# Optimization experiments

Hardware: AMD Instinct MI355X
Metric: run time of the kernel (lower is better)

## Reference

```python
import jax, jax.numpy as jnp
import numpy as np

B = 512        # graphs per batch
N_NODES = 64   # nodes per graph
IN_CH = 256
EMBED = 64
TOPK = 20
NEG_SLOPE = 0.2


def setup_inputs() -> dict:
    key = jax.random.key(0)
    ks = jax.random.split(key, 6)
    N = B * N_NODES
    x = jax.random.normal(ks[0], (N, IN_CH), dtype=jnp.float32)
    # fully-connected graph WITH self loops, per graph, sorted source-major
    src = jnp.repeat(jnp.arange(N_NODES, dtype=jnp.int32), N_NODES)  # [n*n]
    dst = jnp.tile(jnp.arange(N_NODES, dtype=jnp.int32), N_NODES)    # [n*n]
    offs = (jnp.arange(B, dtype=jnp.int32) * N_NODES)[:, None]       # [B,1]
    l = (src[None, :] + offs).reshape(-1)
    r = (dst[None, :] + offs).reshape(-1)
    edge_index = jnp.stack([l, r]).astype(jnp.int32)                 # [2, B*n*n]
    batch = jnp.repeat(jnp.arange(B, dtype=jnp.int32), N_NODES)      # [N]
    glorot = lambda k, sh: jax.random.uniform(k, sh, jnp.float32,
                                              -1.0, 1.0) * np.sqrt(6.0 / (sh[0] + sh[-1]))
    Wl = glorot(ks[1], (EMBED, IN_CH))
    bl = jnp.zeros((EMBED,), jnp.float32)
    Wr = glorot(ks[2], (EMBED, IN_CH))
    br = jnp.zeros((EMBED,), jnp.float32)
    att = glorot(ks[3], (1, EMBED))
    return {"x": x, "edge_index": edge_index, "batch": batch,
            "Wl": Wl, "bl": bl, "Wr": Wr, "br": br, "att": att}


def reference(x, edge_index, batch, Wl, bl, Wr, br, att):
    N = x.shape[0]
    x_l = x @ Wl.T + bl                      # [N, D]
    x_r = x @ Wr.T + br                      # [N, D]
    l, r = edge_index[0], edge_index[1]
    # edge gather + GAT-style score
    e = jax.nn.leaky_relu(x_l[l] + x_r[r], negative_slope=NEG_SLOPE)  # [E, D]
    alpha = (e * att[0]).sum(axis=-1)                                  # [E]
    # segment softmax grouped by source node l (each group is non-empty)
    m = jax.ops.segment_max(alpha, l, num_segments=N)
    a = jnp.exp(alpha - m[l])
    s = jax.ops.segment_sum(a, l, num_segments=N)
    a = a / s[l]
    # kNN sparsify: zero the diagonal then per-row topk
    a3 = a.reshape(B, N_NODES, N_NODES)
    a3 = a3 * (1.0 - jnp.eye(N_NODES, dtype=a3.dtype))
    attention, indices = jax.lax.top_k(a3, TOPK)     # [B, n, k] sorted desc
    attention = attention.reshape(-1)                 # [B*n*k]
    offs = (jnp.arange(B, dtype=jnp.int32) * N_NODES)[:, None]
    index_i = (jnp.repeat(jnp.arange(N_NODES, dtype=jnp.int32), TOPK)[None, :]
               + offs).reshape(-1)
    index_j = (indices.astype(jnp.int32)
               + (jnp.arange(B, dtype=jnp.int32) * N_NODES)[:, None, None]).reshape(-1)
    new_edge_index = jnp.stack([index_i, index_j])    # [2, B*n*k]
    return new_edge_index, attention
```

## Files before the change

kernel.cpp:

```cpp
#include <hip/hip_runtime.h>
#include <stdint.h>

#define NGRAPH 512
#define NN 64
#define INCH 256
#define DD 64
#define TOPK 20
#define XS 68
#define EPR 655360

typedef __attribute__((ext_vector_type(8))) short bf16x8;
typedef __attribute__((ext_vector_type(4))) float f32x4;

static __device__ __forceinline__ uint32_t f2bfbits(float f) {
  uint32_t u = __float_as_uint(f);
  return (u + 0x7FFFu + ((u >> 16) & 1u)) >> 16;
}
static __device__ __forceinline__ uint32_t pk2(float a, float b) {
  return f2bfbits(a) | (f2bfbits(b) << 16);
}

__global__ __launch_bounds__(256) void gat_fused(
    const float* __restrict__ x,
    const float* __restrict__ Wl,
    const float* __restrict__ blv,
    const float* __restrict__ Wr,
    const float* __restrict__ brv,
    const float* __restrict__ att,
    float* __restrict__ out)
{
  __shared__ __align__(16) uint8_t smem[65536];
  __shared__ float attL[DD];
  __shared__ float Sl[NN], Sr[NN];

  uint32_t* Bsh = (uint32_t*)smem;
  float* xlT  = (float*)smem;
  float* xrT  = (float*)(smem + 17408);
  float* alfT = (float*)(smem + 34816);

  const int b    = blockIdx.x;
  const int t    = threadIdx.x;
  const int w    = t >> 6;
  const int lane = t & 63;
  const int quad = lane >> 4;
  const int lo   = lane & 15;
  const int nodeBase = b * NN;

  {
    const int row  = t >> 1;
    const int half = t & 1;
    const float* src = (row < 64) ? (Wl + row * INCH) : (Wr + (row - 64) * INCH);
    uint4* BshV = (uint4*)Bsh;
    #pragma unroll
    for (int q = 0; q < 16; ++q) {
      const int kb = half * 16 + q;
      float4 a = *(const float4*)(src + kb * 8);
      float4 c = *(const float4*)(src + kb * 8 + 4);
      uint4 v = { pk2(a.x, a.y), pk2(a.z, a.w), pk2(c.x, c.y), pk2(c.z, c.w) };
      BshV[row * 32 + (kb ^ (row & 7))] = v;
    }
    if (t < DD) attL[t] = att[t];
  }
  __syncthreads();

  f32x4 acc[8];
  #pragma unroll
  for (int ct = 0; ct < 8; ++ct) acc[ct] = (f32x4){0.f, 0.f, 0.f, 0.f};

  const int r0 = w * 16;
  const uint4* BshV = (const uint4*)Bsh;
  #pragma unroll
  for (int ks = 0; ks < 8; ++ks) {
    const float* ap = x + (size_t)(nodeBase + r0 + lo) * INCH + ks * 32 + quad * 8;
    float4 a0 = *(const float4*)ap;
    float4 a1 = *(const float4*)(ap + 4);
    uint4 au = { pk2(a0.x, a0.y), pk2(a0.z, a0.w), pk2(a1.x, a1.y), pk2(a1.z, a1.w) };
    bf16x8 afrag = __builtin_bit_cast(bf16x8, au);
    #pragma unroll
    for (int ct = 0; ct < 8; ++ct) {
      const int n = (ct & 3) * 16 + lo + ((ct >= 4) ? 64 : 0);
      const int blk = (ks * 4 + quad) ^ (n & 7);
      uint4 bu = BshV[n * 32 + blk];
      bf16x8 bfrag = __builtin_bit_cast(bf16x8, bu);
      acc[ct] = __builtin_amdgcn_mfma_f32_16x16x32_bf16(afrag, bfrag, acc[ct], 0, 0, 0);
    }
  }
  __syncthreads();

  #pragma unroll
  for (int ct = 0; ct < 8; ++ct) {
    const int c = (ct & 3) * 16 + lo;
    const float bias = (ct < 4) ? blv[c] : brv[c];
    float* dstT = (ct < 4) ? xlT : xrT;
    #pragma unroll
    for (int r = 0; r < 4; ++r) {
      const int node = r0 + quad * 4 + r;
      dstT[c * XS + node] = acc[ct][r] + bias;
    }
  }
  __syncthreads();

  if (t < 64) {
    float s = 0.f;
    for (int d = 0; d < DD; ++d) s = fmaf(attL[d], xlT[d * XS + t], s);
    Sl[t] = s;
  } else if (t < 128) {
    const int i = t - 64;
    float s = 0.f;
    for (int d = 0; d < DD; ++d) s = fmaf(attL[d], xrT[d * XS + i], s);
    Sr[i] = s;
  }

  const int i0 = (t >> 4) * 4;
  const int j0 = (t & 15) * 4;
  float pacc[4][4];
  #pragma unroll
  for (int a = 0; a < 4; ++a)
    #pragma unroll
    for (int c = 0; c < 4; ++c) pacc[a][c] = 0.f;

  for (int d = 0; d < DD; ++d) {
    f32x4 xlv = *(const f32x4*)&xlT[d * XS + i0];
    f32x4 xrv = *(const f32x4*)&xrT[d * XS + j0];
    const float ad = attL[d];
    #pragma unroll
    for (int a = 0; a < 4; ++a) {
      #pragma unroll
      for (int c = 0; c < 4; ++c) {
        float s = xlv[a] + xrv[c];
        pacc[a][c] = fmaf(ad, fabsf(s), pacc[a][c]);
      }
    }
  }
  __syncthreads();

  #pragma unroll
  for (int c = 0; c < 4; ++c) {
    f32x4 v;
    #pragma unroll
    for (int a = 0; a < 4; ++a)
      v[a] = 0.6f * (Sl[i0 + a] + Sr[j0 + c]) + 0.4f * pacc[a][c];
    *(f32x4*)&alfT[(j0 + c) * XS + i0] = v;
  }
  __syncthreads();

  if (t < NN) {
    const int i = t;
    float m = -3.4e38f;
    for (int j = 0; j < NN; ++j) m = fmaxf(m, alfT[j * XS + i]);
    float ssum = 0.f;
    for (int j = 0; j < NN; ++j) ssum += __expf(alfT[j * XS + i] - m);
    const float inv = 1.0f / ssum;

    uint32_t tk[TOPK];
    #pragma unroll
    for (int k = 0; k < TOPK; ++k) tk[k] = 0u;

    for (int j = 0; j < NN; ++j) {
      const float av = __expf(alfT[j * XS + i] - m) * inv;
      uint32_t key = (__float_as_uint(av) & 0xFFFFFFC0u) | (uint32_t)(63 - j);
      key = (j == i) ? 0u : key;
      #pragma unroll
      for (int k = TOPK - 1; k >= 1; --k)
        tk[k] = (key > tk[k]) ? ((key < tk[k - 1]) ? key : tk[k - 1]) : tk[k];
      tk[0] = (key > tk[0]) ? key : tk[0];
    }

    const int g = nodeBase + i;
    float vj[TOPK], va[TOPK];
    #pragma unroll
    for (int k = 0; k < TOPK; ++k) {
      const int jj = 63 - (int)(tk[k] & 63u);
      vj[k] = (float)(nodeBase + jj);
      va[k] = __uint_as_float(tk[k] & 0xFFFFFFC0u);
    }

    const float vi = (float)g;
    float4* o0 = (float4*)(out + (size_t)g * 20);
    float4* o1 = (float4*)(out + EPR + (size_t)g * 20);
    float4* o2 = (float4*)(out + 2 * (size_t)EPR + (size_t)g * 20);
    const float4 vi4 = { vi, vi, vi, vi };
    #pragma unroll
    for (int kk = 0; kk < 5; ++kk) {
      o0[kk] = vi4;
      o1[kk] = (float4){ vj[4 * kk], vj[4 * kk + 1], vj[4 * kk + 2], vj[4 * kk + 3] };
      o2[kk] = (float4){ va[4 * kk], va[4 * kk + 1], va[4 * kk + 2], va[4 * kk + 3] };
    }
  }
}

extern "C" void kernel_launch(void* const* d_in, const int* in_sizes, int n_in,
                              void* d_out, int out_size, void* d_ws, size_t ws_size,
                              hipStream_t stream) {
  const float* x   = (const float*)d_in[0];
  const float* Wl  = (const float*)d_in[3];
  const float* bl  = (const float*)d_in[4];
  const float* Wr  = (const float*)d_in[5];
  const float* br  = (const float*)d_in[6];
  const float* att = (const float*)d_in[7];
  gat_fused<<<dim3(NGRAPH), dim3(256), 0, stream>>>(x, Wl, bl, Wr, br, att, (float*)d_out);
}
```

Baseline: 132.0 us.

## Stream weights from global, pack xl/xr as bf16, parallelize top-k across all threads

Drops the shared-memory staging of the bf16 weight matrix and loads and converts Wl/Wr fragments directly from global memory inside the MFMA loop. Stores the projected xl/xr in packed bf16 to shrink shared memory from about 64KB to about 37KB, and sets launch bounds to 4 blocks per SM for higher occupancy. The softmax and top-k now use all 256 threads: each wave handles a 16-column segment and keeps a partial top-16 keyed on raw logits, then 64 threads merge the four lists with a running max/sum and exponentiate only the selected values. The cost is redundant global weight loads and conversions per block, bf16 rounding of intermediates, and a more complex merge.

```diff
diff --git a/kernel.cpp b/kernel.cpp
--- a/kernel.cpp
+++ b/kernel.cpp
@@ -4,13 +4,23 @@
 #define NGRAPH 512
 #define NN 64
 #define INCH 256
-#define DD 64
 #define TOPK 20
-#define XS 68
 #define EPR 655360
 
 typedef __attribute__((ext_vector_type(8))) short bf16x8;
 typedef __attribute__((ext_vector_type(4))) float f32x4;
+typedef __attribute__((ext_vector_type(2))) uint32_t u32x2;
+
+#define XLP   0
+#define XRP   2176
+#define ALF   4352
+#define LISTS 0
+#define MROW  8704
+#define SROW  8960
+#define SLOF  9216
+#define SROF  9280
+#define ATTO  9344
+#define SMEM_DW 9408
 
 static __device__ __forceinline__ uint32_t f2bfbits(float f) {
   uint32_t u = __float_as_uint(f);
@@ -19,8 +29,10 @@
 static __device__ __forceinline__ uint32_t pk2(float a, float b) {
   return f2bfbits(a) | (f2bfbits(b) << 16);
 }
-
-__global__ __launch_bounds__(256) void gat_fused(
+static __device__ __forceinline__ float lo16f(uint32_t p) { return __uint_as_float(p << 16); }
+static __device__ __forceinline__ float hi16f(uint32_t p) { return __uint_as_float(p & 0xFFFF0000u); }
+
+__global__ __launch_bounds__(256, 4) void gat_fused(
     const float* __restrict__ x,
     const float* __restrict__ Wl,
     const float* __restrict__ blv,
@@ -29,14 +41,8 @@
     const float* __restrict__ att,
     float* __restrict__ out)
 {
-  __shared__ __align__(16) uint8_t smem[65536];
-  __shared__ float attL[DD];
-  __shared__ float Sl[NN], Sr[NN];
-
-  uint32_t* Bsh = (uint32_t*)smem;
-  float* xlT  = (float*)smem;
-  float* xrT  = (float*)(smem + 17408);
-  float* alfT = (float*)(smem + 34816);
+  __shared__ __align__(16) uint32_t smemU[SMEM_DW];
+  float* smemF = (float*)smemU;
 
   const int b    = blockIdx.x;
   const int t    = threadIdx.x;
@@ -46,70 +52,56 @@
   const int lo   = lane & 15;
   const int nodeBase = b * NN;
 
-  {
-    const int row  = t >> 1;
-    const int half = t & 1;
-    const float* src = (row < 64) ? (Wl + row * INCH) : (Wr + (row - 64) * INCH);
-    uint4* BshV = (uint4*)Bsh;
-    #pragma unroll
-    for (int q = 0; q < 16; ++q) {
-      const int kb = half * 16 + q;
-      float4 a = *(const float4*)(src + kb * 8);
-      float4 c = *(const float4*)(src + kb * 8 + 4);
-      uint4 v = { pk2(a.x, a.y), pk2(a.z, a.w), pk2(c.x, c.y), pk2(c.z, c.w) };
-      BshV[row * 32 + (kb ^ (row & 7))] = v;
-    }
-    if (t < DD) attL[t] = att[t];
-  }
-  __syncthreads();
+  if (t < 64) smemF[ATTO + t] = att[t];
 
   f32x4 acc[8];
   #pragma unroll
   for (int ct = 0; ct < 8; ++ct) acc[ct] = (f32x4){0.f, 0.f, 0.f, 0.f};
 
   const int r0 = w * 16;
-  const uint4* BshV = (const uint4*)Bsh;
   #pragma unroll
   for (int ks = 0; ks < 8; ++ks) {
-    const float* ap = x + (size_t)(nodeBase + r0 + lo) * INCH + ks * 32 + quad * 8;
+    const int k0 = ks * 32 + quad * 8;
+    const float* ap = x + (size_t)(nodeBase + r0 + lo) * INCH + k0;
     float4 a0 = *(const float4*)ap;
     float4 a1 = *(const float4*)(ap + 4);
     uint4 au = { pk2(a0.x, a0.y), pk2(a0.z, a0.w), pk2(a1.x, a1.y), pk2(a1.z, a1.w) };
     bf16x8 afrag = __builtin_bit_cast(bf16x8, au);
     #pragma unroll
     for (int ct = 0; ct < 8; ++ct) {
-      const int n = (ct & 3) * 16 + lo + ((ct >= 4) ? 64 : 0);
-      const int blk = (ks * 4 + quad) ^ (n & 7);
-      uint4 bu = BshV[n * 32 + blk];
+      const float* wrow = ((ct < 4) ? Wl : Wr) + (size_t)((ct & 3) * 16 + lo) * INCH + k0;
+      float4 b0 = *(const float4*)wrow;
+      float4 b1 = *(const float4*)(wrow + 4);
+      uint4 bu = { pk2(b0.x, b0.y), pk2(b0.z, b0.w), pk2(b1.x, b1.y), pk2(b1.z, b1.w) };
       bf16x8 bfrag = __builtin_bit_cast(bf16x8, bu);
       acc[ct] = __builtin_amdgcn_mfma_f32_16x16x32_bf16(afrag, bfrag, acc[ct], 0, 0, 0);
     }
   }
-  __syncthreads();
 
   #pragma unroll
   for (int ct = 0; ct < 8; ++ct) {
     const int c = (ct & 3) * 16 + lo;
-    const float bias = (ct < 4) ? blv[c] : brv[c];
-    float* dstT = (ct < 4) ? xlT : xrT;
-    #pragma unroll
-    for (int r = 0; r < 4; ++r) {
-      const int node = r0 + quad * 4 + r;
-      dstT[c * XS + node] = acc[ct][r] + bias;
-    }
-  }
-  __syncthreads();
-
-  if (t < 64) {
+    const float bias = ((ct < 4) ? blv : brv)[c];
+    const int base = ((ct < 4) ? XLP : XRP) + c * 34 + (r0 >> 1) + quad * 2;
+    u32x2 v = { pk2(acc[ct][0] + bias, acc[ct][1] + bias),
+                pk2(acc[ct][2] + bias, acc[ct][3] + bias) };
+    *(u32x2*)&smemU[base] = v;
+  }
+  __syncthreads();
+
+  if (t < 128) {
+    const int i = t & 63;
+    const int base = (t < 64) ? XLP : XRP;
     float s = 0.f;
-    for (int d = 0; d < DD; ++d) s = fmaf(attL[d], xlT[d * XS + t], s);
-    Sl[t] = s;
-  } else if (t < 128) {
-    const int i = t - 64;
-    float s = 0.f;
-    for (int d = 0; d < DD; ++d) s = fmaf(attL[d], xrT[d * XS + i], s);
-    Sr[i] = s;
-  }
+    #pragma unroll 4
+    for (int d = 0; d < 64; ++d) {
+      uint32_t p = smemU[base + d * 34 + (i >> 1)];
+      float v = (i & 1) ? hi16f(p) : lo16f(p);
+      s = fmaf(smemF[ATTO + d], v, s);
+    }
+    smemF[((t < 64) ? SLOF : SROF) + i] = s;
+  }
+  __syncthreads();
 
   const int i0 = (t >> 4) * 4;
   const int j0 = (t & 15) * 4;
@@ -119,62 +111,115 @@
     #pragma unroll
     for (int c = 0; c < 4; ++c) pacc[a][c] = 0.f;
 
-  for (int d = 0; d < DD; ++d) {
-    f32x4 xlv = *(const f32x4*)&xlT[d * XS + i0];
-    f32x4 xrv = *(const f32x4*)&xrT[d * XS + j0];
-    const float ad = attL[d];
+  #pragma unroll 4
+  for (int d = 0; d < 64; ++d) {
+    u32x2 pl = *(const u32x2*)&smemU[XLP + d * 34 + (i0 >> 1)];
+    u32x2 pr = *(const u32x2*)&smemU[XRP + d * 34 + (j0 >> 1)];
+    const float ad = smemF[ATTO + d];
+    float xl[4] = { lo16f(pl.x), hi16f(pl.x), lo16f(pl.y), hi16f(pl.y) };
+    float xr[4] = { lo16f(pr.x), hi16f(pr.x), lo16f(pr.y), hi16f(pr.y) };
     #pragma unroll
     for (int a = 0; a < 4; ++a) {
       #pragma unroll
       for (int c = 0; c < 4; ++c) {
-        float s = xlv[a] + xrv[c];
+        float s = xl[a] + xr[c];
         pacc[a][c] = fmaf(ad, fabsf(s), pacc[a][c]);
       }
     }
   }
-  __syncthreads();
-
-  #pragma unroll
-  for (int c = 0; c < 4; ++c) {
-    f32x4 v;
-    #pragma unroll
-    for (int a = 0; a < 4; ++a)
-      v[a] = 0.6f * (Sl[i0 + a] + Sr[j0 + c]) + 0.4f * pacc[a][c];
-    *(f32x4*)&alfT[(j0 + c) * XS + i0] = v;
-  }
-  __syncthreads();
-
-  if (t < NN) {
-    const int i = t;
-    float m = -3.4e38f;
-    for (int j = 0; j < NN; ++j) m = fmaxf(m, alfT[j * XS + i]);
-    float ssum = 0.f;
-    for (int j = 0; j < NN; ++j) ssum += __expf(alfT[j * XS + i] - m);
-    const float inv = 1.0f / ssum;
-
-    uint32_t tk[TOPK];
-    #pragma unroll
-    for (int k = 0; k < TOPK; ++k) tk[k] = 0u;
-
-    for (int j = 0; j < NN; ++j) {
-      const float av = __expf(alfT[j * XS + i] - m) * inv;
-      uint32_t key = (__float_as_uint(av) & 0xFFFFFFC0u) | (uint32_t)(63 - j);
-      key = (j == i) ? 0u : key;
+  {
+    f32x4 srv = *(const f32x4*)&smemF[SROF + j0];
+    #pragma unroll
+    for (int a = 0; a < 4; ++a) {
+      const float sl = smemF[SLOF + i0 + a];
+      f32x4 v;
       #pragma unroll
-      for (int k = TOPK - 1; k >= 1; --k)
+      for (int c = 0; c < 4; ++c)
+        v[c] = 0.6f * (sl + srv[c]) + 0.4f * pacc[a][c];
+      *(f32x4*)&smemF[ALF + (i0 + a) * 68 + j0] = v;
+    }
+  }
+  __syncthreads();
+
+  {
+    const int row = t & 63;
+    const int seg = t >> 6;
+    const int segBase = seg * 16;
+    float fr[16];
+    *(f32x4*)&fr[0]  = *(const f32x4*)&smemF[ALF + row * 68 + segBase];
+    *(f32x4*)&fr[4]  = *(const f32x4*)&smemF[ALF + row * 68 + segBase + 4];
+    *(f32x4*)&fr[8]  = *(const f32x4*)&smemF[ALF + row * 68 + segBase + 8];
+    *(f32x4*)&fr[12] = *(const f32x4*)&smemF[ALF + row * 68 + segBase + 12];
+
+    float mp = fr[0];
+    #pragma unroll
+    for (int e = 1; e < 16; ++e) mp = fmaxf(mp, fr[e]);
+    float sp = 0.f;
+    #pragma unroll
+    for (int e = 0; e < 16; ++e) sp += __expf(fr[e] - mp);
+
+    uint32_t tk[16];
+    #pragma unroll
+    for (int k = 0; k < 16; ++k) tk[k] = 0u;
+    #pragma unroll
+    for (int e = 0; e < 16; ++e) {
+      const int j = segBase + e;
+      uint32_t u = __float_as_uint(fr[e]);
+      uint32_t key = u ^ ((uint32_t)((int32_t)u >> 31) | 0x80000000u);
+      key = (key & 0xFFFFFFC0u) | (uint32_t)(63 - j);
+      key = (j == row) ? 0u : key;
+      #pragma unroll
+      for (int k = 15; k >= 1; --k)
         tk[k] = (key > tk[k]) ? ((key < tk[k - 1]) ? key : tk[k - 1]) : tk[k];
       tk[0] = (key > tk[0]) ? key : tk[0];
     }
-
-    const int g = nodeBase + i;
-    float vj[TOPK], va[TOPK];
+    #pragma unroll
+    for (int k = 0; k < 16; ++k)
+      smemU[LISTS + row * 65 + segBase + k] = tk[k];
+    smemF[MROW + seg * 64 + row] = mp;
+    smemF[SROW + seg * 64 + row] = sp;
+  }
+  __syncthreads();
+
+  if (t < 64) {
+    const int row = t;
+    const int lb = LISTS + row * 65;
+    float m01 = fmaxf(smemF[MROW + row], smemF[MROW + 64 + row]);
+    float m23 = fmaxf(smemF[MROW + 128 + row], smemF[MROW + 192 + row]);
+    float m = fmaxf(m01, m23);
+    float S = 0.f;
+    #pragma unroll
+    for (int p = 0; p < 4; ++p)
+      S += smemF[SROW + p * 64 + row] * __expf(smemF[MROW + p * 64 + row] - m);
+    const float invS = 1.0f / S;
+
+    uint32_t h0 = smemU[lb + 0], h1 = smemU[lb + 16], h2 = smemU[lb + 32], h3 = smemU[lb + 48];
+    int p0 = 0, p1 = 0, p2 = 0, p3 = 0;
+    float va[TOPK], vj[TOPK];
+
     #pragma unroll
     for (int k = 0; k < TOPK; ++k) {
-      const int jj = 63 - (int)(tk[k] & 63u);
-      vj[k] = (float)(nodeBase + jj);
-      va[k] = __uint_as_float(tk[k] & 0xFFFFFFC0u);
-    }
-
+      uint32_t k01 = (h0 > h1) ? h0 : h1;
+      uint32_t k23 = (h2 > h3) ? h2 : h3;
+      uint32_t key = (k01 > k23) ? k01 : k23;
+      const int wsel = (key == h0) ? 0 : (key == h1) ? 1 : (key == h2) ? 2 : 3;
+
+      uint32_t ub = (key & 0x80000000u) ? (key ^ 0x80000000u) : ~key;
+      float alpha = __uint_as_float(ub & 0xFFFFFFC0u);
+      const int j = 63 - (int)(key & 63u);
+      va[k] = __expf(alpha - m) * invS;
+      vj[k] = (float)(nodeBase + j);
+
+      int np = ((wsel == 0) ? p0 : (wsel == 1) ? p1 : (wsel == 2) ? p2 : p3) + 1;
+      uint32_t hn = (np < 16) ? smemU[lb + wsel * 16 + np] : 0u;
+      p0 += (wsel == 0); p1 += (wsel == 1); p2 += (wsel == 2); p3 += (wsel == 3);
+      h0 = (wsel == 0) ? hn : h0;
+      h1 = (wsel == 1) ? hn : h1;
+      h2 = (wsel == 2) ? hn : h2;
+      h3 = (wsel == 3) ? hn : h3;
+    }
+
+    const int g = nodeBase + row;
     const float vi = (float)g;
     float4* o0 = (float4*)(out + (size_t)g * 20);
     float4* o1 = (float4*)(out + EPR + (size_t)g * 20);
```

Result: slower. 138.6 us (+5.0%).
